# Kernel optimization log

Measured on AMD Instinct MI355X. Metric: run time of the kernel, lower is better.

The kernel has to match this reference:

```python
import jax, jax.numpy as jnp
import numpy as np

NQ = 6          # num_qubits
BS = 3          # basis_size (Pauli x,y,z)
HID = 32        # LSTM hidden size
SNAPS = 16      # max_num_snapshots
BATCH = 1024
DIM = 2 ** NQ   # 64


def _pauli():
    sx = np.array([[0., 1.], [1., 0.]], dtype=np.complex64)
    sy = np.array([[0., -1j], [1j, 0.]], dtype=np.complex64)
    sz = np.array([[1., 0.], [0., -1.]], dtype=np.complex64)
    return np.stack([sx, sy, sz], axis=0)


def setup_inputs():
    key = jax.random.key(0)
    ks = jax.random.split(key, 12)
    snapshot = jax.random.uniform(ks[0], (BATCH, NQ), jnp.float32, -1.0, 1.0)
    basis_comp_vector = jax.nn.softmax(
        jax.random.normal(ks[1], (BATCH, NQ, BS), jnp.float32), axis=-1)
    # valid density matrices: rho = A A^dag / tr
    ar = jax.random.normal(ks[2], (BATCH, DIM, DIM), jnp.float32)
    ai = jax.random.normal(ks[3], (BATCH, DIM, DIM), jnp.float32)
    A = ar + 1j * ai
    rho_c = jnp.einsum('bij,bkj->bik', A, jnp.conj(A))
    tr = jnp.trace(rho_c, axis1=1, axis2=2)[:, None, None]
    rho_c = rho_c / tr
    rho = jnp.stack([jnp.real(rho_c), jnp.imag(rho_c)], axis=1).astype(jnp.float32)
    h0 = jax.random.normal(ks[4], (BATCH, HID), jnp.float32)
    c0 = jax.random.normal(ks[5], (BATCH, HID), jnp.float32)
    in_dim = NQ + NQ * BS
    W_ih = jax.random.normal(ks[6], (4 * HID, in_dim), jnp.float32) * 0.1
    W_hh = jax.random.normal(ks[7], (4 * HID, HID), jnp.float32) * 0.1
    b_ih = jax.random.normal(ks[8], (4 * HID,), jnp.float32) * 0.05
    b_hh = jax.random.normal(ks[9], (4 * HID,), jnp.float32) * 0.05
    Wp = jax.random.normal(ks[10], (NQ, HID, BS), jnp.float32) * 0.1
    bp = jax.random.normal(ks[11], (NQ, BS), jnp.float32) * 0.05
    pauli = _pauli()
    basis_r = jnp.asarray(np.real(pauli), jnp.float32)
    basis_i = jnp.asarray(np.imag(pauli), jnp.float32)
    return {"snapshot": snapshot, "basis_comp_vector": basis_comp_vector,
            "rho": rho, "h0": h0, "c0": c0,
            "W_ih": W_ih, "W_hh": W_hh, "b_ih": b_ih, "b_hh": b_hh,
            "Wp": Wp, "bp": bp, "basis_r": basis_r, "basis_i": basis_i}


def _apply(p, M, axis, b):
    # apply 2x2 batched operator M [b,2,2] on tensor axis `axis` of p [b]+(2,)*2NQ
    pm = jnp.moveaxis(p, axis, 1)
    shp = pm.shape
    out = jnp.einsum('bij,bjr->bir', M, pm.reshape(b, 2, -1)).reshape(shp)
    return jnp.moveaxis(out, 1, axis)


def _measure(rho_t, probs, basis, basis_c, b):
    # sequential single-qubit measurement on the collapsing mixed state
    pc = probs.astype(jnp.complex64)
    M = jnp.einsum('bqs,sij->bqij', pc, basis)    # prob-mixed basis ops
    Mc = jnp.einsum('bqs,sij->bqij', pc, basis_c)
    p = rho_t
    outs = []
    for q in range(NQ):
        p = _apply(p, M[:, q], 1 + q, b)          # row index of qubit q
        p = _apply(p, Mc[:, q], 1 + NQ + q, b)    # col index of qubit q
        tr = jnp.trace(p.reshape(b, DIM, DIM), axis1=1, axis2=2)
        outs.append(jnp.real(tr))                 # measurement value s
        p = p / tr.reshape((b,) + (1,) * (2 * NQ))  # renormalized post-state
    return jnp.stack(outs, axis=1)                 # [b, NQ]


def _forward(snapshot, basis_comp_vector, rho, h0, c0,
             W_ih, W_hh, b_ih, b_hh, Wp, bp, basis_r, basis_i):
    b = snapshot.shape[0]
    basis = (basis_r + 1j * basis_i).astype(jnp.complex64)
    basis_c = jnp.conj(basis)
    rho_t = (rho[:, 0] + 1j * rho[:, 1]).astype(jnp.complex64)
    rho_t = rho_t.reshape((b,) + (2,) * (2 * NQ))

    x = jnp.concatenate([snapshot, basis_comp_vector.reshape(b, -1)], axis=-1)
    feats = [x]
    h, c = h0, c0
    for _ in range(SNAPS - 1):
        # torch LSTMCell: gate order i, f, g, o
        g = x @ W_ih.T + b_ih + h @ W_hh.T + b_hh
        gi, gf, gg, go = jnp.split(g, 4, axis=-1)
        c = jax.nn.sigmoid(gf) * c + jax.nn.sigmoid(gi) * jnp.tanh(gg)
        h = jax.nn.sigmoid(go) * jnp.tanh(c)
        probs = jax.nn.softmax(jnp.einsum('bh,qhs->bqs', h, Wp) + bp, axis=-1)
        # torch.Tensor(snapshot_batch) detaches -> stop_gradient
        snaps = jax.lax.stop_gradient(_measure(rho_t, probs, basis, basis_c, b))
        x = jnp.concatenate([snaps, probs.reshape(b, -1)], axis=-1)
        feats.append(x)

    # classical-shadow reconstruction: kron_q (I + 3 s_q B_q)/2, averaged
    eye2 = jnp.eye(2, dtype=jnp.complex64)
    acc = jnp.zeros((b, DIM, DIM), jnp.complex64)
    last_bv = None
    for xw in feats:
        shadow = xw[:, :NQ]
        bv = xw[:, NQ:].reshape(b, NQ, BS)
        last_bv = bv
        Bq = jnp.einsum('bqs,sij->bqij', bv.astype(jnp.complex64), basis)
        rc = (eye2 + 3.0 * shadow[:, :, None, None].astype(jnp.complex64) * Bq) / 2.0
        k = rc[:, 0]
        dd = 2
        for q in range(1, NQ):  # batched kron chain
            k = jnp.einsum('bij,bkl->bikjl', k, rc[:, q]).reshape(b, dd * 2, dd * 2)
            dd *= 2
        acc = acc + k
    rho_rec = acc / SNAPS
    out = jnp.stack([jnp.real(rho_rec), jnp.imag(rho_rec)], axis=1)
    return out, last_bv


def reference(snapshot, basis_comp_vector, rho, h0, c0,
              W_ih, W_hh, b_ih, b_hh, Wp, bp, basis_r, basis_i):
    return _forward(snapshot, basis_comp_vector, rho, h0, c0,
                    W_ih, W_hh, b_ih, b_hh, Wp, bp, basis_r, basis_i)
```

## Files before the change

kernel.cpp:

```cpp
#include <hip/hip_runtime.h>

#define NQ 6
#define HID 32
#define SNAPS 16
#define BATCH 1024
#define FSTRIDE 24
#define FTOT 384
#define KSTR 24
#define KF   192

typedef float vfloat4 __attribute__((ext_vector_type(4)));

__device__ __forceinline__ float sigm_f(float x) { return 1.0f / (1.0f + __expf(-x)); }
__device__ __forceinline__ float tanh_f(float x) { return 1.0f - 2.0f / (__expf(2.0f * x) + 1.0f); }

__device__ __forceinline__ void rc_entry(float g, float b0, float b1, float b2,
                                         int i, int j, float& re, float& im) {
    if (i == j) { re = 0.5f + (i ? -g * b2 : g * b2); im = 0.0f; }
    else        { re = g * b0;  im = (i ? g * b1 : -g * b1); }
}

__global__ __launch_bounds__(256, 2)
void fused_kernel(const float* __restrict__ snapshot,
                  const float* __restrict__ bcv,
                  const float* __restrict__ h0,
                  const float* __restrict__ c0,
                  const float* __restrict__ W_ih,
                  const float* __restrict__ W_hh,
                  const float* __restrict__ b_ih,
                  const float* __restrict__ b_hh,
                  const float* __restrict__ Wp,
                  const float* __restrict__ bp,
                  float* __restrict__ out,
                  float* __restrict__ out_tail)
{
    __shared__ __align__(16) float sKA[16 * KF];
    __shared__ __align__(16) float sKB[16 * KF];
    __shared__ __align__(16) float feat[FTOT];
    __shared__ __align__(16) float sh[HID];
    __shared__ __align__(16) float sg[128];

    const int b = blockIdx.x;
    const int t = threadIdx.x;

    float4 wih[6], whh[8];
    float bias = 0.0f;
    if (t < 128) {
        const float4* p = (const float4*)(W_ih + t * 24);
        #pragma unroll
        for (int k = 0; k < 6; ++k) wih[k] = p[k];
        const float4* q = (const float4*)(W_hh + t * 32);
        #pragma unroll
        for (int k = 0; k < 8; ++k) whh[k] = q[k];
        bias = b_ih[t] + b_hh[t];
    }
    float wp[32];
    float bpv = 0.0f, c = 0.0f;
    if (t < 18) {
        int q = t / 3, s = t - 3 * q;
        #pragma unroll
        for (int k = 0; k < 32; ++k) wp[k] = Wp[q * 96 + 3 * k + s];
        bpv = bp[t];
    }
    if (t < 32) { c = c0[b * 32 + t]; sh[t] = h0[b * 32 + t]; }
    if (t < 24) feat[t] = (t < 6) ? snapshot[b * 6 + t] : bcv[b * 18 + (t - 6)];
    __syncthreads();

    for (int step = 0; step < SNAPS - 1; ++step) {
        if (t < 128) {
            const float4* x4 = (const float4*)(feat + step * FSTRIDE);
            const float4* h4 = (const float4*)sh;
            float ga = bias, gb = 0.0f;
            #pragma unroll
            for (int k = 0; k < 6; ++k) {
                float4 xq = x4[k];
                ga += xq.x * wih[k].x + xq.y * wih[k].y;
                gb += xq.z * wih[k].z + xq.w * wih[k].w;
            }
            #pragma unroll
            for (int k = 0; k < 8; ++k) {
                float4 hq = h4[k];
                ga += hq.x * whh[k].x + hq.y * whh[k].y;
                gb += hq.z * whh[k].z + hq.w * whh[k].w;
            }
            sg[t] = ga + gb;
        }
        __syncthreads();

        if (t < 64) {
            if (t < 32) {
                float gi = sg[t], gf = sg[32 + t], gg = sg[64 + t], go = sg[96 + t];
                c = sigm_f(gf) * c + sigm_f(gi) * tanh_f(gg);
                sh[t] = sigm_f(go) * tanh_f(c);
            }
            __builtin_amdgcn_wave_barrier();
            float logit = bpv;
            const float4* h4b = (const float4*)sh;
            #pragma unroll
            for (int k = 0; k < 8; ++k) {
                float4 hq = h4b[k];
                logit += hq.x * wp[4 * k] + hq.y * wp[4 * k + 1]
                       + hq.z * wp[4 * k + 2] + hq.w * wp[4 * k + 3];
            }
            int q3 = 3 * (t < 6 ? t : 0);
            float l0 = __shfl(logit, q3), l1 = __shfl(logit, q3 + 1), l2 = __shfl(logit, q3 + 2);
            if (t < 6) {
                float m = fmaxf(l0, fmaxf(l1, l2));
                float e0 = __expf(l0 - m), e1 = __expf(l1 - m), e2 = __expf(l2 - m);
                float inv = 1.0f / (e0 + e1 + e2);
                float p0 = e0 * inv, p1 = e1 * inv, p2 = e2 * inv;
                float snap = p0 * p0 + p1 * p1 + p2 * p2;
                float* fd = feat + (step + 1) * FSTRIDE;
                fd[t] = snap;
                fd[6 + 3 * t]     = p0;
                fd[6 + 3 * t + 1] = p1;
                fd[6 + 3 * t + 2] = p2;
            }
        }
        __syncthreads();
    }

    if (t < 18) out_tail[b * 18 + t] = feat[15 * FSTRIDE + 6 + t];

    for (int n = t; n < 2048; n += 256) {
        int f = n >> 7, r = n & 127;
        int half = r >> 6, a = r & 63;
        const float* fx = &feat[f * FSTRIDE];
        int i0 = (a >> 5) & 1, i1 = (a >> 4) & 1, i2 = (a >> 3) & 1;
        int j0 = (a >> 2) & 1, j1 = (a >> 1) & 1, j2 = a & 1;
        int q = 3 * half;
        float g0 = 1.5f * fx[q], g1 = 1.5f * fx[q + 1], g2 = 1.5f * fx[q + 2];
        const float* bb = fx + 6 + 3 * q;
        float r0, m0, r1, m1, r2, m2;
        rc_entry(g0, bb[0], bb[1], bb[2], i0, j0, r0, m0);
        rc_entry(g1, bb[3], bb[4], bb[5], i1, j1, r1, m1);
        rc_entry(g2, bb[6], bb[7], bb[8], i2, j2, r2, m2);
        float pr = r0 * r1 - m0 * m1, pi = r0 * m1 + m0 * r1;
        float qr = pr * r2 - pi * m2, qi = pr * m2 + pi * r2;
        int row = a >> 3, col = a & 7;
        if (half == 0) {
            int off = f * KF + col * KSTR + ((row & 1) ? (7 + row) : row);
            sKA[off] = qr; sKA[off + 1] = qi;
        } else {
            int off = f * KF + row * KSTR + 2 * col;
            sKB[off] = qr; sKB[off + 1] = qi;
        }
    }
    __syncthreads();

    const int u = t & 15, v = t >> 4;
    const float* baseA = sKA + (u >> 1) * KSTR + 8 * (v >> 3);
    const float* baseB = sKB + (v & 7) * KSTR + 8 * (u & 1);
    float accr[4][4], acci[4][4];
    #pragma unroll
    for (int e = 0; e < 4; ++e)
        #pragma unroll
        for (int d = 0; d < 4; ++d) { accr[e][d] = 0.0f; acci[e][d] = 0.0f; }

    #pragma unroll 2
    for (int f = 0; f < SNAPS; ++f) {
        float4 A0 = *(const float4*)(baseA + f * KF);
        float4 A1 = *(const float4*)(baseA + f * KF + 4);
        float4 B0 = *(const float4*)(baseB + f * KF);
        float4 B1 = *(const float4*)(baseB + f * KF + 4);
        float ar[4] = {A0.x, A0.z, A1.x, A1.z};
        float ai[4] = {A0.y, A0.w, A1.y, A1.w};
        float br[4] = {B0.x, B0.z, B1.x, B1.z};
        float bi[4] = {B0.y, B0.w, B1.y, B1.w};
        #pragma unroll
        for (int e = 0; e < 4; ++e)
            #pragma unroll
            for (int d = 0; d < 4; ++d) {
                accr[e][d] += ar[e] * br[d] - ai[e] * bi[d];
                acci[e][d] += ar[e] * bi[d] + ai[e] * br[d];
            }
    }

    const float s = 1.0f / 16.0f;
    float* outb = out + (size_t)b * 8192;
    #pragma unroll
    for (int e = 0; e < 4; ++e) {
        int i = v + 16 * e;
        vfloat4 r4 = { accr[e][0] * s, accr[e][1] * s, accr[e][2] * s, accr[e][3] * s };
        vfloat4 i4 = { acci[e][0] * s, acci[e][1] * s, acci[e][2] * s, acci[e][3] * s };
        __builtin_nontemporal_store(r4, (vfloat4*)(outb + i * 64 + 4 * u));
        __builtin_nontemporal_store(i4, (vfloat4*)(outb + 4096 + i * 64 + 4 * u));
    }
}

extern "C" void kernel_launch(void* const* d_in, const int* in_sizes, int n_in,
                              void* d_out, int out_size, void* d_ws, size_t ws_size,
                              hipStream_t stream) {
    const float* snapshot = (const float*)d_in[0];
    const float* bcv      = (const float*)d_in[1];
    const float* h0       = (const float*)d_in[3];
    const float* c0       = (const float*)d_in[4];
    const float* W_ih     = (const float*)d_in[5];
    const float* W_hh     = (const float*)d_in[6];
    const float* b_ih     = (const float*)d_in[7];
    const float* b_hh     = (const float*)d_in[8];
    const float* Wp       = (const float*)d_in[9];
    const float* bp       = (const float*)d_in[10];
    float* out = (float*)d_out;

    fused_kernel<<<BATCH, 256, 0, stream>>>(
        snapshot, bcv, h0, c0, W_ih, W_hh, b_ih, b_hh, Wp, bp,
        out, out + (size_t)BATCH * 8192);
}
```

Baseline: 131.0 us.

## Split fused kernel into LSTM kernel and reconstruction kernel via output scratch

Splits the single fused kernel in two. A 128-thread LSTM kernel runs the serial recurrence and writes its 384 features per batch into the start of that batch's output slot. A separate 256-thread reconstruction kernel then reads those features back and builds the Kronecker-product output in place. The aim is to avoid idling half the threads during the LSTM loop and to let each phase get its own occupancy, using higher launch bounds for recon. It also splits the dot-product accumulators to shorten dependency chains. The cost is an extra launch and a global round-trip, plus an in-place dependency: each recon block reads feats from the output region it later overwrites, which works only because the read happens before the __syncthreads that precedes its writes.

```diff
diff --git a/kernel.cpp b/kernel.cpp
--- a/kernel.cpp
+++ b/kernel.cpp
@@ -20,22 +20,20 @@
     else        { re = g * b0;  im = (i ? g * b1 : -g * b1); }
 }
 
-__global__ __launch_bounds__(256, 2)
-void fused_kernel(const float* __restrict__ snapshot,
-                  const float* __restrict__ bcv,
-                  const float* __restrict__ h0,
-                  const float* __restrict__ c0,
-                  const float* __restrict__ W_ih,
-                  const float* __restrict__ W_hh,
-                  const float* __restrict__ b_ih,
-                  const float* __restrict__ b_hh,
-                  const float* __restrict__ Wp,
-                  const float* __restrict__ bp,
-                  float* __restrict__ out,
-                  float* __restrict__ out_tail)
+__global__ __launch_bounds__(128, 2)
+void lstm_kernel(const float* __restrict__ snapshot,
+                 const float* __restrict__ bcv,
+                 const float* __restrict__ h0,
+                 const float* __restrict__ c0,
+                 const float* __restrict__ W_ih,
+                 const float* __restrict__ W_hh,
+                 const float* __restrict__ b_ih,
+                 const float* __restrict__ b_hh,
+                 const float* __restrict__ Wp,
+                 const float* __restrict__ bp,
+                 float* __restrict__ feat_scratch,
+                 float* __restrict__ out_tail)
 {
-    __shared__ __align__(16) float sKA[16 * KF];
-    __shared__ __align__(16) float sKB[16 * KF];
     __shared__ __align__(16) float feat[FTOT];
     __shared__ __align__(16) float sh[HID];
     __shared__ __align__(16) float sg[128];
@@ -44,16 +42,16 @@
     const int t = threadIdx.x;
 
     float4 wih[6], whh[8];
-    float bias = 0.0f;
-    if (t < 128) {
+    {
         const float4* p = (const float4*)(W_ih + t * 24);
         #pragma unroll
         for (int k = 0; k < 6; ++k) wih[k] = p[k];
         const float4* q = (const float4*)(W_hh + t * 32);
         #pragma unroll
         for (int k = 0; k < 8; ++k) whh[k] = q[k];
-        bias = b_ih[t] + b_hh[t];
-    }
+    }
+    const float bias = b_ih[t] + b_hh[t];
+
     float wp[32];
     float bpv = 0.0f, c = 0.0f;
     if (t < 18) {
@@ -67,10 +65,10 @@
     __syncthreads();
 
     for (int step = 0; step < SNAPS - 1; ++step) {
-        if (t < 128) {
+        {
             const float4* x4 = (const float4*)(feat + step * FSTRIDE);
             const float4* h4 = (const float4*)sh;
-            float ga = bias, gb = 0.0f;
+            float ga = bias, gb = 0.0f, gc = 0.0f, gd = 0.0f;
             #pragma unroll
             for (int k = 0; k < 6; ++k) {
                 float4 xq = x4[k];
@@ -80,10 +78,10 @@
             #pragma unroll
             for (int k = 0; k < 8; ++k) {
                 float4 hq = h4[k];
-                ga += hq.x * whh[k].x + hq.y * whh[k].y;
-                gb += hq.z * whh[k].z + hq.w * whh[k].w;
-            }
-            sg[t] = ga + gb;
+                gc += hq.x * whh[k].x + hq.y * whh[k].y;
+                gd += hq.z * whh[k].z + hq.w * whh[k].w;
+            }
+            sg[t] = (ga + gb) + (gc + gd);
         }
         __syncthreads();
 
@@ -94,14 +92,21 @@
                 sh[t] = sigm_f(go) * tanh_f(c);
             }
             __builtin_amdgcn_wave_barrier();
-            float logit = bpv;
+            float lg0 = bpv, lg1 = 0.0f;
             const float4* h4b = (const float4*)sh;
             #pragma unroll
-            for (int k = 0; k < 8; ++k) {
+            for (int k = 0; k < 4; ++k) {
                 float4 hq = h4b[k];
-                logit += hq.x * wp[4 * k] + hq.y * wp[4 * k + 1]
-                       + hq.z * wp[4 * k + 2] + hq.w * wp[4 * k + 3];
-            }
+                lg0 += hq.x * wp[4 * k] + hq.y * wp[4 * k + 1]
+                     + hq.z * wp[4 * k + 2] + hq.w * wp[4 * k + 3];
+            }
+            #pragma unroll
+            for (int k = 4; k < 8; ++k) {
+                float4 hq = h4b[k];
+                lg1 += hq.x * wp[4 * k] + hq.y * wp[4 * k + 1]
+                     + hq.z * wp[4 * k + 2] + hq.w * wp[4 * k + 3];
+            }
+            float logit = lg0 + lg1;
             int q3 = 3 * (t < 6 ? t : 0);
             float l0 = __shfl(logit, q3), l1 = __shfl(logit, q3 + 1), l2 = __shfl(logit, q3 + 2);
             if (t < 6) {
@@ -120,7 +125,25 @@
         __syncthreads();
     }
 
+    if (t < 96)
+        ((float4*)(feat_scratch + (size_t)b * 8192))[t] = ((const float4*)feat)[t];
     if (t < 18) out_tail[b * 18 + t] = feat[15 * FSTRIDE + 6 + t];
+}
+
+__global__ __launch_bounds__(256, 4)
+void recon_kernel(const float* feat_src,
+                  float* out)
+{
+    __shared__ __align__(16) float sKA[16 * KF];
+    __shared__ __align__(16) float sKB[16 * KF];
+    __shared__ __align__(16) float feat[FTOT];
+
+    const int b = blockIdx.x;
+    const int t = threadIdx.x;
+
+    if (t < 96)
+        ((float4*)feat)[t] = ((const float4*)(feat_src + (size_t)b * 8192))[t];
+    __syncthreads();
 
     for (int n = t; n < 2048; n += 256) {
         int f = n >> 7, r = n & 127;
@@ -203,7 +226,8 @@
     const float* bp       = (const float*)d_in[10];
     float* out = (float*)d_out;
 
-    fused_kernel<<<BATCH, 256, 0, stream>>>(
+    lstm_kernel<<<BATCH, 128, 0, stream>>>(
         snapshot, bcv, h0, c0, W_ih, W_hh, b_ih, b_hh, Wp, bp,
-        out, out + (size_t)BATCH * 8192);
-}
+        out , out + (size_t)BATCH * 8192 );
+    recon_kernel<<<BATCH, 256, 0, stream>>>(out, out);
+}
```

New measurement: 135.1 us. 3.2% more time.
